# Kernel optimization log

Hardware: AMD Instinct MI355X
Metric: run time of the kernel (lower is better)

## Reference

```python
import jax, jax.numpy as jnp
import numpy as np

N = 50000      # nodes
E = 800000     # edges (before self loops)
D_IN = 128
D_H = 128
HEADS = 4
C = D_H // HEADS
D_OUT = 64
G = 50         # graphs in batch
EPS = 1e-5


def setup_inputs() -> dict:
    key = jax.random.key(0)
    ks = jax.random.split(key, 40)
    def rn(k, shape, scale=0.05):
        return jax.random.normal(k, shape, jnp.float32) * scale
    inp = {}
    inp['x'] = jax.random.normal(ks[0], (N, D_IN), jnp.float32)
    inp['edge_index'] = jax.random.randint(ks[1], (2, E), 0, N, dtype=jnp.int32)
    inp['batch'] = jnp.sort(jax.random.randint(ks[2], (N,), 0, G, dtype=jnp.int32))
    # GATConv 1 (in=D_IN, heads=4, out-per-head=C, concat)
    inp['gat1_W'] = rn(ks[3], (D_IN, D_H))
    inp['gat1_as'] = rn(ks[4], (HEADS, C))
    inp['gat1_ad'] = rn(ks[5], (HEADS, C))
    inp['gat1_b'] = rn(ks[6], (D_H,))
    # GATConv 2 (in=D_H)
    inp['gat2_W'] = rn(ks[7], (D_H, D_H))
    inp['gat2_as'] = rn(ks[8], (HEADS, C))
    inp['gat2_ad'] = rn(ks[9], (HEADS, C))
    inp['gat2_b'] = rn(ks[10], (D_H,))
    # SAGEConv 3/4/5: lin_l (aggregated neighbors, has bias), lin_r (root, no bias)
    for i, kk in zip((3, 4, 5), (11, 14, 17)):
        inp[f'sage{i}_Wl'] = rn(ks[kk], (D_H, D_H))
        inp[f'sage{i}_bl'] = rn(ks[kk + 1], (D_H,))
        inp[f'sage{i}_Wr'] = rn(ks[kk + 2], (D_H, D_H))
    # BatchNorms (training-mode batch statistics)
    for i in range(1, 6):
        inp[f'bn{i}_g'] = jnp.ones((D_H,), jnp.float32)
        inp[f'bn{i}_b'] = jnp.zeros((D_H,), jnp.float32)
    # residual projections + final fc
    inp['res1_W'] = rn(ks[20], (D_IN, D_H)); inp['res1_b'] = rn(ks[21], (D_H,))
    inp['res2_W'] = rn(ks[22], (D_H, D_H)); inp['res2_b'] = rn(ks[23], (D_H,))
    inp['fc_W'] = rn(ks[24], (D_H, D_OUT)); inp['fc_b'] = rn(ks[25], (D_OUT,))
    return inp


def _segsum(v, idx, n):
    return jax.ops.segment_sum(v, idx, num_segments=n)


def _gat(x, W, a_src, a_dst, b, src, dst):
    # PyG GATConv with self loops already appended to (src, dst).
    h = (x @ W).reshape(N, HEADS, C)
    es = jnp.einsum('nhc,hc->nh', h, a_src)           # [N,H]
    ed = jnp.einsum('nhc,hc->nh', h, a_dst)
    e = jax.nn.leaky_relu(es[src] + ed[dst], 0.2)     # [Etot,H]
    m = jax.ops.segment_max(e, dst, num_segments=N)
    m = jnp.where(jnp.isfinite(m), m, 0.0)
    w = jnp.exp(e - m[dst])
    z = _segsum(w, dst, N)
    alpha = w / jnp.maximum(z[dst], 1e-16)            # edge softmax over dst
    out = _segsum(h[src] * alpha[:, :, None], dst, N)  # [N,H,C]
    return out.reshape(N, D_H) + b


def _sage(x, Wl, bl, Wr, src, dst):
    # PyG SAGEConv(aggr='mean'): lin_l(mean_neighbors) + lin_r(x)
    deg = _segsum(jnp.ones((src.shape[0],), x.dtype), dst, N)
    mean = _segsum(x[src], dst, N) / jnp.maximum(deg, 1.0)[:, None]
    return mean @ Wl + bl + x @ Wr


def _bn(x, g, b):
    mu = x.mean(0)
    var = x.var(0)
    return g * (x - mu) * jax.lax.rsqrt(var + EPS) + b


def reference(x, edge_index, batch,
              gat1_W, gat1_as, gat1_ad, gat1_b,
              gat2_W, gat2_as, gat2_ad, gat2_b,
              sage3_Wl, sage3_bl, sage3_Wr,
              sage4_Wl, sage4_bl, sage4_Wr,
              sage5_Wl, sage5_bl, sage5_Wr,
              bn1_g, bn1_b, bn2_g, bn2_b, bn3_g, bn3_b, bn4_g, bn4_b, bn5_g, bn5_b,
              res1_W, res1_b, res2_W, res2_b, fc_W, fc_b):
    src, dst = edge_index[0], edge_index[1]
    loops = jnp.arange(N, dtype=edge_index.dtype)
    gsrc = jnp.concatenate([src, loops])   # GATConv adds self loops by default
    gdst = jnp.concatenate([dst, loops])
    lrelu = lambda v: jax.nn.leaky_relu(v, 0.2)

    res1 = x @ res1_W + res1_b
    h = _gat(x, gat1_W, gat1_as, gat1_ad, gat1_b, gsrc, gdst)
    h = lrelu(_bn(h, bn1_g, bn1_b) + res1)            # dropout = identity (eval)

    res2 = h @ res2_W + res2_b
    h = _gat(h, gat2_W, gat2_as, gat2_ad, gat2_b, gsrc, gdst)
    h = lrelu(_bn(h, bn2_g, bn2_b) + res2)

    h = lrelu(_bn(_sage(h, sage3_Wl, sage3_bl, sage3_Wr, src, dst), bn3_g, bn3_b))
    h = lrelu(_bn(_sage(h, sage4_Wl, sage4_bl, sage4_Wr, src, dst), bn4_g, bn4_b))
    h = lrelu(_bn(_sage(h, sage5_Wl, sage5_bl, sage5_Wr, src, dst), bn5_g, bn5_b))

    # global_mean_pool over graphs
    cnt = jax.ops.segment_sum(jnp.ones((N,), h.dtype), batch, num_segments=G)
    pooled = jax.ops.segment_sum(h, batch, num_segments=G) / jnp.maximum(cnt, 1.0)[:, None]
    return pooled @ fc_W + fc_b
```

## Files before the change

### kernel.cpp

```cpp
#include <hip/hip_runtime.h>
#include <math.h>
#include <stdint.h>

#define N_NODES 50000
#define N_EDGES 800000
#define D 128
#define GR 50
#define EPSV 1e-5f

typedef __attribute__((ext_vector_type(8))) short bf16x8;
typedef __attribute__((ext_vector_type(4))) float f32x4;

__device__ __forceinline__ float lrelu(float v){ return v > 0.f ? v : 0.2f*v; }

__device__ __forceinline__ unsigned int f2bf(float f){
  union { float f; uint32_t i; } v; v.f = f;
  uint32_t r = v.i + 0x7fffu + ((v.i >> 16) & 1u);
  return r >> 16;
}
__device__ __forceinline__ float2 bf2f2(uint32_t u){
  union { uint32_t i; float f; } a, b;
  a.i = u << 16;
  b.i = u & 0xffff0000u;
  return make_float2(a.f, b.f);
}

__global__ void k_countrank(const int* __restrict__ dst, int* __restrict__ deg,
                            int* __restrict__ rank){
  int e = blockIdx.x*256 + threadIdx.x;
  if (e < N_EDGES) rank[e] = atomicAdd(&deg[dst[e]], 1);
}
__global__ void k_scan1(const int* __restrict__ deg, int* __restrict__ bsum){
  __shared__ int s[256];
  int i = blockIdx.x*256 + threadIdx.x;
  int v = (i < N_NODES) ? deg[i] : 0;
  s[threadIdx.x] = v; __syncthreads();
  for (int off = 128; off > 0; off >>= 1){
    if (threadIdx.x < off) s[threadIdx.x] += s[threadIdx.x + off];
    __syncthreads();
  }
  if (threadIdx.x == 0) bsum[blockIdx.x] = s[0];
}
__global__ void k_scan2b(int* __restrict__ bsum, int nb, int* __restrict__ rowStart){
  __shared__ int s[256];
  int t = threadIdx.x;
  int v = (t < nb) ? bsum[t] : 0;
  s[t] = v; __syncthreads();
  for (int off = 1; off < 256; off <<= 1){
    int xv = (t >= off) ? s[t - off] : 0;
    __syncthreads();
    s[t] += xv;
    __syncthreads();
  }
  if (t < nb) bsum[t] = s[t] - v;
  if (t == 255) rowStart[N_NODES] = s[255];
}
__global__ void k_scan3(const int* __restrict__ deg, const int* __restrict__ bsum,
                        int* __restrict__ rowStart){
  __shared__ int s[256];
  int i = blockIdx.x*256 + threadIdx.x;
  int v = (i < N_NODES) ? deg[i] : 0;
  s[threadIdx.x] = v; __syncthreads();
  for (int off = 1; off < 256; off <<= 1){
    int xv = (threadIdx.x >= off) ? s[threadIdx.x - off] : 0;
    __syncthreads();
    s[threadIdx.x] += xv;
    __syncthreads();
  }
  if (i < N_NODES) rowStart[i] = bsum[blockIdx.x] + s[threadIdx.x] - v;
}
__global__ void k_scatter(const int* __restrict__ src, const int* __restrict__ dst,
                          const int* __restrict__ rank, const int* __restrict__ rowStart,
                          int* __restrict__ srcList){
  int e = blockIdx.x*256 + threadIdx.x;
  if (e < N_EDGES)
    srcList[rowStart[dst[e]] + rank[e]] = src[e];
}

__global__ void k_cast_x(const float* __restrict__ x, unsigned short* __restrict__ x16){
  int idx = blockIdx.x*256 + threadIdx.x;
  if (idx >= N_NODES*32) return;
  float4 v = *(const float4*)(x + (size_t)idx*4);
  uint2 pk;
  pk.x = f2bf(v.x) | (f2bf(v.y) << 16);
  pk.y = f2bf(v.z) | (f2bf(v.w) << 16);
  *(uint2*)(x16 + (size_t)idx*4) = pk;
}

struct WPack { const float* w[10]; };
__global__ void k_castw(WPack p, unsigned short* __restrict__ wt){
  int mat = blockIdx.x >> 6;
  int local = (blockIdx.x & 63)*256 + threadIdx.x;
  int c = local >> 7, k = local & 127;
  wt[(size_t)mat*16384 + c*128 + k] = (unsigned short)f2bf(p.w[mat][k*128 + c]);
}

__device__ __forceinline__ void stage_w(const unsigned short* __restrict__ wt,
                                        unsigned short* __restrict__ lds, int t){
  #pragma unroll
  for (int i = 0; i < 8; ++i){
    int ch = i*256 + t;
    int col = ch >> 4, kc = ch & 15;
    *(uint4*)(&lds[col*136 + kc*8]) = *(const uint4*)(wt + ((size_t)col << 7) + (kc << 3));
  }
}

__device__ __forceinline__ void load_a(const unsigned short* __restrict__ xrow,
                                       int quad, bf16x8 a[4]){
  #pragma unroll
  for (int ks = 0; ks < 4; ++ks)
    a[ks] = *(const bf16x8*)(xrow + ks*32 + quad*8);
}

__device__ __forceinline__ void mfma_regs(const bf16x8 a[4],
                                          const unsigned short* __restrict__ lds,
                                          int lane, f32x4 acc[8]){
  int quad = lane >> 4, m = lane & 15;
  #pragma unroll
  for (int ks = 0; ks < 4; ++ks){
    #pragma unroll
    for (int nt = 0; nt < 8; ++nt){
      bf16x8 b = *(const bf16x8*)(&lds[(nt*16 + m)*136 + ks*32 + quad*8]);
      acc[nt] = __builtin_amdgcn_mfma_f32_16x16x32_bf16(a[ks], b, acc[nt], 0, 0, 0);
    }
  }
}

__device__ __forceinline__ void epi_store16(f32x4 acc[8], const float* bias,
    unsigned short* __restrict__ ldsw, unsigned short* __restrict__ Y16,
    int rbase, int lane, int n){
  int quad = lane >> 4, m = lane & 15;
  #pragma unroll
  for (int nt = 0; nt < 8; ++nt){
    int col = nt*16 + m;
    float bv = bias ? bias[col] : 0.f;
    #pragma unroll
    for (int reg = 0; reg < 4; ++reg)
      ldsw[(quad*4 + reg)*132 + col] = (unsigned short)f2bf(acc[nt][reg] + bv);
  }
  int r = lane >> 2, seg = lane & 3;
  int grow = rbase + r;
  if (grow < n){
    unsigned short* gp = Y16 + (size_t)grow*128 + seg*32;
    #pragma unroll
    for (int j = 0; j < 4; ++j)
      *(uint4*)(gp + j*8) = *(const uint4*)(&ldsw[r*132 + seg*32 + j*8]);
  }
}

__global__ __launch_bounds__(256) void k_mgemm_dual(const unsigned short* __restrict__ X16,
    const unsigned short* __restrict__ wtres, const unsigned short* __restrict__ wtgat,
    const float* __restrict__ bres, const float* __restrict__ as_,
    const float* __restrict__ ad_, unsigned short* __restrict__ R16,
    unsigned short* __restrict__ H16, float* __restrict__ es, float* __restrict__ ed,
    int n){
  __shared__ __align__(16) unsigned short Wlds[128*136];
  int t = threadIdx.x, lane = t & 63, w = t >> 6;
  int quad = lane >> 4, m = lane & 15;
  int rbase = blockIdx.x*64 + w*16;
  int rowA = rbase + m; if (rowA >= n) rowA = n - 1;
  bf16x8 a[4];
  load_a(X16 + (size_t)rowA*128, quad, a);
  stage_w(wtres, Wlds, t);
  f32x4 accR[8], accG[8];
  #pragma unroll
  for (int nt = 0; nt < 8; ++nt){
    accR[nt][0]=0.f; accR[nt][1]=0.f; accR[nt][2]=0.f; accR[nt][3]=0.f;
    accG[nt][0]=0.f; accG[nt][1]=0.f; accG[nt][2]=0.f; accG[nt][3]=0.f;
  }
  __syncthreads();
  mfma_regs(a, Wlds, lane, accR);
  __syncthreads();
  stage_w(wtgat, Wlds, t);
  __syncthreads();
  mfma_regs(a, Wlds, lane, accG);

  float asv[8], adv[8];
  #pragma unroll
  for (int nt = 0; nt < 8; ++nt){ asv[nt] = as_[nt*16 + m]; adv[nt] = ad_[nt*16 + m]; }
  #pragma unroll
  for (int reg = 0; reg < 4; ++reg){
    int row = rbase + quad*4 + reg;
    float pe[4], pd[4];
    #pragma unroll
    for (int h = 0; h < 4; ++h){
      pe[h] = accG[2*h][reg]*asv[2*h] + accG[2*h+1][reg]*asv[2*h+1];
      pd[h] = accG[2*h][reg]*adv[2*h] + accG[2*h+1][reg]*adv[2*h+1];
    }
    #pragma unroll
    for (int h = 0; h < 4; ++h){
      pe[h] += __shfl_xor(pe[h], 1); pe[h] += __shfl_xor(pe[h], 2);
      pe[h] += __shfl_xor(pe[h], 4); pe[h] += __shfl_xor(pe[h], 8);
      pd[h] += __shfl_xor(pd[h], 1); pd[h] += __shfl_xor(pd[h], 2);
      pd[h] += __shfl_xor(pd[h], 4); pd[h] += __shfl_xor(pd[h], 8);
    }
    if (m == 0 && row < n){
      #pragma unroll
      for (int h = 0; h < 4; ++h){ es[row*4 + h] = pe[h]; ed[row*4 + h] = pd[h]; }
    }
  }
  __syncthreads();
  epi_store16(accR, bres,    Wlds + w*2112, R16, rbase, lane, n);
  epi_store16(accG, nullptr, Wlds + w*2112, H16, rbase, lane, n);
}

__global__ __launch_bounds__(256) void k_mgemm2(const unsigned short* __restrict__ Xa,
    const unsigned short* __restrict__ wta, const unsigned short* __restrict__ Xb,
    const unsigned short* __restrict__ wtb, const float* __restrict__ bias,
    unsigned short* __restrict__ Y16, int n, float* __restrict__ bnpart){
  __shared__ __align__(16) unsigned short Wlds[128*136];
  __shared__ float wredS[4][128], wredQ[4][128];
  int t = threadIdx.x, lane = t & 63, w = t >> 6;
  int quad = lane >> 4, m = lane & 15;
  int rbase = blockIdx.x*64 + w*16;
  int rowA = rbase + m; if (rowA >= n) rowA = n - 1;
  bf16x8 aa[4], ab[4];
  load_a(Xa + (size_t)rowA*128, quad, aa);
  load_a(Xb + (size_t)rowA*128, quad, ab);
  stage_w(wta, Wlds, t);
  f32x4 acc[8];
  #pragma unroll
  for (int nt = 0; nt < 8; ++nt){ acc[nt][0]=0.f; acc[nt][1]=0.f; acc[nt][2]=0.f; acc[nt][3]=0.f; }
  __syncthreads();
  mfma_regs(aa, Wlds, lane, acc);
  __syncthreads();
  stage_w(wtb, Wlds, t);
  __syncthreads();
  mfma_regs(ab, Wlds, lane, acc);

  float colS[8], colQ[8];
  #pragma unroll
  for (int nt = 0; nt < 8; ++nt){
    float bv = bias[nt*16 + m];
    float s = 0.f, q = 0.f;
    #pragma unroll
    for (int reg = 0; reg < 4; ++reg){
      float o = acc[nt][reg] + bv;
      acc[nt][reg] = o;
      if (rbase + quad*4 + reg < n){ s += o; q += o*o; }
    }
    s += __shfl_xor(s, 16); s += __shfl_xor(s, 32);
    q += __shfl_xor(q, 16); q += __shfl_xor(q, 32);
    colS[nt] = s; colQ[nt] = q;
  }
  if (quad == 0){
    #pragma unroll
    for (int nt = 0; nt < 8; ++nt){
      wredS[w][nt*16 + m] = colS[nt];
      wredQ[w][nt*16 + m] = colQ[nt];
    }
  }
  __syncthreads();
  if (t < 128){
    float S = wredS[0][t] + wredS[1][t] + wredS[2][t] + wredS[3][t];
    float Q = wredQ[0][t] + wredQ[1][t] + wredQ[2][t] + wredQ[3][t];
    bnpart[(size_t)blockIdx.x*256 + t]       = S;
    bnpart[(size_t)blockIdx.x*256 + 128 + t] = Q;
  }
  epi_store16(acc, nullptr, Wlds + w*2112, Y16, rbase, lane, n);
}

__global__ void k_bnred(const float* __restrict__ part, int nblk,
                        float* __restrict__ sums){
  int g = blockIdx.x, t = threadIdx.x;
  int chunk = (nblk + 63) / 64;
  int b0 = g*chunk, b1 = min(nblk, b0 + chunk);
  float s = 0.f;
  for (int b = b0; b < b1; ++b) s += part[(size_t)b*256 + t];
  if (b0 < b1) atomicAdd(&sums[t], s);
}

__global__ __launch_bounds__(256) void k_gat(const uint4* __restrict__ h16,
    const float* __restrict__ es, const float* __restrict__ edv,
    const int* __restrict__ rowStart, const int* __restrict__ srcList,
    const float* __restrict__ bias, uint4* __restrict__ out16){
  int i = blockIdx.x*4 + (threadIdx.x >> 6);
  if (i >= N_NODES) return;
  int lane = threadIdx.x & 63;
  int sub = lane >> 4;
  int m   = lane & 15;
  int hd  = m >> 2;
  float edi = edv[i*4 + hd];
  float acc[8];
  #pragma unroll
  for (int j = 0; j < 8; ++j) acc[j] = 0.f;
  float z = 0.f;
  if (sub == 0){
    float ws = __expf(lrelu(es[i*4 + hd] + edi));
    uint4 u = h16[i*16 + m];
    float2 v0=bf2f2(u.x), v1=bf2f2(u.y), v2=bf2f2(u.z), v3=bf2f2(u.w);
    acc[0]=v0.x*ws; acc[1]=v0.y*ws; acc[2]=v1.x*ws; acc[3]=v1.y*ws;
    acc[4]=v2.x*ws; acc[5]=v2.y*ws; acc[6]=v3.x*ws; acc[7]=v3.y*ws;
    z = ws;
  }
  int k0 = rowStart[i], ke = rowStart[i + 1];
  for (int k = k0; k < ke; k += 8){
    int e0 = k + sub, e1 = k + 4 + sub;
    int c0 = e0 < ke ? e0 : ke - 1;
    int c1 = e1 < ke ? e1 : ke - 1;
    int s0 = srcList[c0];
    int s1 = srcList[c1];
    uint4 u0 = h16[s0*16 + m];
    uint4 u1 = h16[s1*16 + m];
    float w0 = (e0 < ke) ? __expf(lrelu(es[s0*4 + hd] + edi)) : 0.f;
    float w1 = (e1 < ke) ? __expf(lrelu(es[s1*4 + hd] + edi)) : 0.f;
    z += w0 + w1;
    float2 a0=bf2f2(u0.x), a1=bf2f2(u0.y), a2=bf2f2(u0.z), a3=bf2f2(u0.w);
    float2 b0=bf2f2(u1.x), b1=bf2f2(u1.y), b2=bf2f2(u1.z), b3=bf2f2(u1.w);
    acc[0] += a0.x*w0 + b0.x*w1;  acc[1] += a0.y*w0 + b0.y*w1;
    acc[2] += a1.x*w0 + b1.x*w1;  acc[3] += a1.y*w0 + b1.y*w1;
    acc[4] += a2.x*w0 + b2.x*w1;  acc[5] += a2.y*w0 + b2.y*w1;
    acc[6] += a3.x*w0 + b3.x*w1;  acc[7] += a3.y*w0 + b3.y*w1;
  }
  #pragma unroll
  for (int j = 0; j < 8; ++j){
    acc[j] += __shfl_xor(acc[j], 16);
    acc[j] += __shfl_xor(acc[j], 32);
  }
  z += __shfl_xor(z, 16);
  z += __shfl_xor(z, 32);
  if (sub == 0){
    float inv = 1.f / z;
    float4 bv0 = *(const float4*)(bias + m*8);
    float4 bv1 = *(const float4*)(bias + m*8 + 4);
    uint4 pk;
    pk.x = f2bf(acc[0]*inv + bv0.x) | (f2bf(acc[1]*inv + bv0.y) << 16);
    pk.y = f2bf(acc[2]*inv + bv0.z) | (f2bf(acc[3]*inv + bv0.w) << 16);
    pk.z = f2bf(acc[4]*inv + bv1.x) | (f2bf(acc[5]*inv + bv1.y) << 16);
    pk.w = f2bf(acc[6]*inv + bv1.z) | (f2bf(acc[7]*inv + bv1.w) << 16);
    out16[i*16 + m] = pk;
  }
}

__global__ __launch_bounds__(256) void k_sage_mean(const uint4* __restrict__ h16,
    const int* __restrict__ rowStart, const int* __restrict__ srcList,
    uint4* __restrict__ out16){
  int i = blockIdx.x*4 + (threadIdx.x >> 6);
  if (i >= N_NODES) return;
  int lane = threadIdx.x & 63;
  int sub = lane >> 4;
  int m   = lane & 15;
  float acc[8];
  #pragma unroll
  for (int j = 0; j < 8; ++j) acc[j] = 0.f;
  int k0 = rowStart[i], ke = rowStart[i + 1];
  for (int k = k0; k < ke; k += 8){
    int e0 = k + sub, e1 = k + 4 + sub;
    int c0 = e0 < ke ? e0 : ke - 1;
    int c1 = e1 < ke ? e1 : ke - 1;
    int s0 = srcList[c0];
    int s1 = srcList[c1];
    uint4 u0 = h16[s0*16 + m];
    uint4 u1 = h16[s1*16 + m];
    float w0 = (e0 < ke) ? 1.f : 0.f;
    float w1 = (e1 < ke) ? 1.f : 0.f;
    float2 a0=bf2f2(u0.x), a1=bf2f2(u0.y), a2=bf2f2(u0.z), a3=bf2f2(u0.w);
    float2 b0=bf2f2(u1.x), b1=bf2f2(u1.y), b2=bf2f2(u1.z), b3=bf2f2(u1.w);
    acc[0] += a0.x*w0 + b0.x*w1;  acc[1] += a0.y*w0 + b0.y*w1;
    acc[2] += a1.x*w0 + b1.x*w1;  acc[3] += a1.y*w0 + b1.y*w1;
    acc[4] += a2.x*w0 + b2.x*w1;  acc[5] += a2.y*w0 + b2.y*w1;
    acc[6] += a3.x*w0 + b3.x*w1;  acc[7] += a3.y*w0 + b3.y*w1;
  }
  #pragma unroll
  for (int j = 0; j < 8; ++j){
    acc[j] += __shfl_xor(acc[j], 16);
    acc[j] += __shfl_xor(acc[j], 32);
  }
  if (sub == 0){
    int dg = ke - k0;
    float inv = 1.f / (float)(dg > 0 ? dg : 1);
    uint4 pk;
    pk.x = f2bf(acc[0]*inv) | (f2bf(acc[1]*inv) << 16);
    pk.y = f2bf(acc[2]*inv) | (f2bf(acc[3]*inv) << 16);
    pk.z = f2bf(acc[4]*inv) | (f2bf(acc[5]*inv) << 16);
    pk.w = f2bf(acc[6]*inv) | (f2bf(acc[7]*inv) << 16);
    out16[i*16 + m] = pk;
  }
}

__global__ __launch_bounds__(256) void k_bnstat(const unsigned int* __restrict__ x16,
                                                float* __restrict__ sums){
  int colu = threadIdx.x & 63;
  int ro   = threadIdx.x >> 6;
  float s0 = 0.f, s1 = 0.f, q0 = 0.f, q1 = 0.f;
  for (int r = blockIdx.x*4 + ro; r < N_NODES; r += gridDim.x*4){
    float2 v = bf2f2(x16[(size_t)r*64 + colu]);
    s0 += v.x; s1 += v.y; q0 += v.x*v.x; q1 += v.y*v.y;
  }
  __shared__ float rs0[256], rs1[256], rq0[256], rq1[256];
  int t = threadIdx.x;
  rs0[t] = s0; rs1[t] = s1; rq0[t] = q0; rq1[t] = q1;
  __syncthreads();
  if (t < 64){
    float S0 = rs0[t] + rs0[t+64] + rs0[t+128] + rs0[t+192];
    float S1 = rs1[t] + rs1[t+64] + rs1[t+128] + rs1[t+192];
    float Q0 = rq0[t] + rq0[t+64] + rq0[t+128] + rq0[t+192];
    float Q1 = rq1[t] + rq1[t+64] + rq1[t+128] + rq1[t+192];
    atomicAdd(&sums[2*t],       S0);
    atomicAdd(&sums[2*t + 1],   S1);
    atomicAdd(&sums[128 + 2*t],     Q0);
    atomicAdd(&sums[128 + 2*t + 1], Q1);
  }
}

__global__ void k_bnapply(const unsigned int* __restrict__ x16,
    const float* __restrict__ sums, const float* __restrict__ g,
    const float* __restrict__ b, const unsigned int* __restrict__ res16,
    unsigned int* __restrict__ y16){
  int f = blockIdx.x*256 + threadIdx.x;
  if (f >= N_NODES*32) return;
  int c = (f & 31) * 4;
  uint2 u = *(const uint2*)(x16 + (size_t)f*2);
  float2 vA = bf2f2(u.x), vB = bf2f2(u.y);
  float vv[4] = {vA.x, vA.y, vB.x, vB.y};
  float rr[4] = {0.f, 0.f, 0.f, 0.f};
  if (res16){
    uint2 ur = *(const uint2*)(res16 + (size_t)f*2);
    float2 rA = bf2f2(ur.x), rB = bf2f2(ur.y);
    rr[0]=rA.x; rr[1]=rA.y; rr[2]=rB.x; rr[3]=rB.y;
  }
  float o[4];
  const float invn = 1.f / (float)N_NODES;
  #pragma unroll
  for (int j = 0; j < 4; ++j){
    int cc = c + j;
    float mu  = sums[cc] * invn;
    float var = sums[128 + cc] * invn - mu*mu;
    float rs  = rsqrtf(var + EPSV);
    o[j] = lrelu((vv[j] - mu)*rs*g[cc] + b[cc] + rr[j]);
  }
  uint2 pk;
  pk.x = f2bf(o[0]) | (f2bf(o[1]) << 16);
  pk.y = f2bf(o[2]) | (f2bf(o[3]) << 16);
  *(uint2*)(y16 + (size_t)f*2) = pk;
}

__global__ __launch_bounds__(256) void k_pool(const unsigned int* __restrict__ h16,
    const int* __restrict__ batch, float* __restrict__ pooled,
    float* __restrict__ cnt){
  int colu = threadIdx.x & 63;
  int ro   = threadIdx.x >> 6;
  int base = blockIdx.x * 128;
  int g_cur = -1; float a0 = 0.f, a1 = 0.f, cacc = 0.f;
  for (int ii = 0; ii < 32; ++ii){
    int r = base + ro + ii*4;
    if (r >= N_NODES) break;
    int g = batch[r];
    if (g != g_cur){
      if (g_cur >= 0){
        atomicAdd(&pooled[g_cur*D + 2*colu],     a0);
        atomicAdd(&pooled[g_cur*D + 2*colu + 1], a1);
        if (colu == 0) atomicAdd(&cnt[g_cur], cacc);
      }
      a0 = 0.f; a1 = 0.f; cacc = 0.f; g_cur = g;
    }
    float2 v = bf2f2(h16[(size_t)r*64 + colu]);
    a0 += v.x; a1 += v.y; cacc += 1.f;
  }
  if (g_cur >= 0){
    atomicAdd(&pooled[g_cur*D + 2*colu],     a0);
    atomicAdd(&pooled[g_cur*D + 2*colu + 1], a1);
    if (colu == 0) atomicAdd(&cnt[g_cur], cacc);
  }
}

__global__ void k_fc(const float* __restrict__ pooled, const float* __restrict__ cnt,
    const float* __restrict__ W, const float* __restrict__ b, float* __restrict__ out){
  int idx = blockIdx.x*256 + threadIdx.x;
  if (idx >= GR*64) return;
  int g = idx >> 6, o = idx & 63;
  const float* p = pooled + g*D;
  float s = 0.f;
  for (int c2 = 0; c2 < D; ++c2) s += p[c2] * W[c2*64 + o];
  float inv = 1.f / fmaxf(cnt[g], 1.f);
  out[idx] = s*inv + b[o];
}

extern "C" void kernel_launch(void* const* d_in, const int* in_sizes, int n_in,
                              void* d_out, int out_size, void* d_ws, size_t ws_size,
                              hipStream_t stream){
  (void)in_sizes; (void)n_in; (void)out_size; (void)ws_size;
  const float* x       = (const float*)d_in[0];
  const int*   ei      = (const int*)  d_in[1];
  const int*   batch   = (const int*)  d_in[2];
  const float* gat1_W  = (const float*)d_in[3];
  const float* gat1_as = (const float*)d_in[4];
  const float* gat1_ad = (const float*)d_in[5];
  const float* gat1_b  = (const float*)d_in[6];
  const float* gat2_W  = (const float*)d_in[7];
  const float* gat2_as = (const float*)d_in[8];
  const float* gat2_ad = (const float*)d_in[9];
  const float* gat2_b  = (const float*)d_in[10];
  const float* s3_Wl   = (const float*)d_in[11];
  const float* s3_bl   = (const float*)d_in[12];
  const float* s3_Wr   = (const float*)d_in[13];
  const float* s4_Wl   = (const float*)d_in[14];
  const float* s4_bl   = (const float*)d_in[15];
  const float* s4_Wr   = (const float*)d_in[16];
  const float* s5_Wl   = (const float*)d_in[17];
  const float* s5_bl   = (const float*)d_in[18];
  const float* s5_Wr   = (const float*)d_in[19];
  const float* bn1_g = (const float*)d_in[20]; const float* bn1_b = (const float*)d_in[21];
  const float* bn2_g = (const float*)d_in[22]; const float* bn2_b = (const float*)d_in[23];
  const float* bn3_g = (const float*)d_in[24]; const float* bn3_b = (const float*)d_in[25];
  const float* bn4_g = (const float*)d_in[26]; const float* bn4_b = (const float*)d_in[27];
  const float* bn5_g = (const float*)d_in[28]; const float* bn5_b = (const float*)d_in[29];
  const float* res1_W = (const float*)d_in[30]; const float* res1_b = (const float*)d_in[31];
  const float* res2_W = (const float*)d_in[32]; const float* res2_b = (const float*)d_in[33];
  const float* fc_W   = (const float*)d_in[34]; const float* fc_b   = (const float*)d_in[35];
  float* out = (float*)d_out;

  char* ws = (char*)d_ws;
  size_t off = 0;
  auto alloc = [&](size_t bytes) -> void* {
    void* p = ws + off; off += (bytes + 255) & ~(size_t)255; return p;
  };
  const int mgrid = (N_NODES + 63) / 64;
  int*   rowStart = (int*)  alloc((N_NODES + 1) * 4);
  int*   deg      = (int*)  alloc((size_t)N_NODES * 4);
  int*   rank     = (int*)  alloc((size_t)N_EDGES * 4);
  int*   srcList  = (int*)  alloc((size_t)N_EDGES * 4);
  int*   bsum     = (int*)  alloc(256 * 4);
  float* bnsums   = (float*)alloc(5 * 256 * 4);
  float* pooled   = (float*)alloc(GR * D * 4);
  float* cnt      = (float*)alloc(64 * 4);
  float* es       = (float*)alloc((size_t)N_NODES * 4 * 4);
  float* edv      = (float*)alloc((size_t)N_NODES * 4 * 4);
  float* bnpart   = (float*)alloc((size_t)mgrid * 256 * 4);
  unsigned short* Wt16 = (unsigned short*)alloc(10 * 16384 * 2);
  unsigned short* HX   = (unsigned short*)alloc((size_t)N_NODES * D * 2);
  unsigned short* H16a = (unsigned short*)alloc((size_t)N_NODES * D * 2);
  unsigned short* HO   = (unsigned short*)alloc((size_t)N_NODES * D * 2);
  unsigned short* HR   = (unsigned short*)alloc((size_t)N_NODES * D * 2);

  const int* srcE = ei;
  const int* dstE = ei + N_EDGES;
  const int nb = (N_NODES + 255) / 256;
  const int egrid = (N_EDGES + 255) / 256;
  const int agrid = (N_NODES + 3) / 4;
  const int bgrid = (N_NODES*32 + 255) / 256;
  const int pgrid = (N_NODES + 127) / 128;

  hipMemsetAsync(deg, 0, (size_t)N_NODES*4, stream);
  hipMemsetAsync(bnsums, 0, (5*256 + GR*D + 64)*4, stream);
  k_countrank<<<egrid, 256, 0, stream>>>(dstE, deg, rank);
  k_scan1<<<nb, 256, 0, stream>>>(deg, bsum);
  k_scan2b<<<1, 256, 0, stream>>>(bsum, nb, rowStart);
  k_scan3<<<nb, 256, 0, stream>>>(deg, bsum, rowStart);
  k_scatter<<<egrid, 256, 0, stream>>>(srcE, dstE, rank, rowStart, srcList);

  WPack wp;
  wp.w[0]=res1_W; wp.w[1]=gat1_W; wp.w[2]=res2_W; wp.w[3]=gat2_W;
  wp.w[4]=s3_Wl;  wp.w[5]=s3_Wr;  wp.w[6]=s4_Wl;  wp.w[7]=s4_Wr;
  wp.w[8]=s5_Wl;  wp.w[9]=s5_Wr;
  k_castw<<<640, 256, 0, stream>>>(wp, Wt16);
  k_cast_x<<<bgrid, 256, 0, stream>>>(x, HX);

  k_mgemm_dual<<<mgrid, 256, 0, stream>>>(HX, Wt16 + 0*16384, Wt16 + 1*16384,
                                          res1_b, gat1_as, gat1_ad,
                                          HR, H16a, es, edv, N_NODES);
  k_gat<<<agrid, 256, 0, stream>>>((const uint4*)H16a, es, edv, rowStart,
                                   srcList, gat1_b, (uint4*)HO);
  k_bnstat<<<256, 256, 0, stream>>>((const unsigned int*)HO, bnsums);
  k_bnapply<<<bgrid, 256, 0, stream>>>((const unsigned int*)HO, bnsums, bn1_g, bn1_b,
                                       (const unsigned int*)HR, (unsigned int*)H16a);

  k_mgemm_dual<<<mgrid, 256, 0, stream>>>(H16a, Wt16 + 2*16384, Wt16 + 3*16384,
                                          res2_b, gat2_as, gat2_ad,
                                          HR, HX, es, edv, N_NODES);
  k_gat<<<agrid, 256, 0, stream>>>((const uint4*)HX, es, edv, rowStart,
                                   srcList, gat2_b, (uint4*)HO);
  k_bnstat<<<256, 256, 0, stream>>>((const unsigned int*)HO, bnsums + 256);
  k_bnapply<<<bgrid, 256, 0, stream>>>((const unsigned int*)HO, bnsums + 256, bn2_g, bn2_b,
                                       (const unsigned int*)HR, (unsigned int*)H16a);

  k_sage_mean<<<agrid, 256, 0, stream>>>((const uint4*)H16a, rowStart, srcList,
                                         (uint4*)HX);
  k_mgemm2<<<mgrid, 256, 0, stream>>>(HX, Wt16 + 4*16384, H16a, Wt16 + 5*16384,
                                      s3_bl, HO, N_NODES, bnpart);
  k_bnred<<<64, 256, 0, stream>>>(bnpart, mgrid, bnsums + 512);
  k_bnapply<<<bgrid, 256, 0, stream>>>((const unsigned int*)HO, bnsums + 512, bn3_g, bn3_b,
                                       nullptr, (unsigned int*)H16a);

  k_sage_mean<<<agrid, 256, 0, stream>>>((const uint4*)H16a, rowStart, srcList,
                                         (uint4*)HX);
  k_mgemm2<<<mgrid, 256, 0, stream>>>(HX, Wt16 + 6*16384, H16a, Wt16 + 7*16384,
                                      s4_bl, HO, N_NODES, bnpart);
  k_bnred<<<64, 256, 0, stream>>>(bnpart, mgrid, bnsums + 768);
  k_bnapply<<<bgrid, 256, 0, stream>>>((const unsigned int*)HO, bnsums + 768, bn4_g, bn4_b,
                                       nullptr, (unsigned int*)H16a);

  k_sage_mean<<<agrid, 256, 0, stream>>>((const uint4*)H16a, rowStart, srcList,
                                         (uint4*)HX);
  k_mgemm2<<<mgrid, 256, 0, stream>>>(HX, Wt16 + 8*16384, H16a, Wt16 + 9*16384,
                                      s5_bl, HO, N_NODES, bnpart);
  k_bnred<<<64, 256, 0, stream>>>(bnpart, mgrid, bnsums + 1024);
  k_bnapply<<<bgrid, 256, 0, stream>>>((const unsigned int*)HO, bnsums + 1024, bn5_g, bn5_b,
                                       nullptr, (unsigned int*)H16a);

  k_pool<<<pgrid, 256, 0, stream>>>((const unsigned int*)H16a, batch, pooled, cnt);
  k_fc<<<(GR*64 + 255)/256, 256, 0, stream>>>(pooled, cnt, fc_W, fc_b, out);
}
```

Measured before the change: 614.7 us.

## Merge cast kernels, fuse pool with fc, peel gather tail, single memset

Combines the weight and input bf16 cast kernels into one launch. Fuses global mean pooling with the final fc using a last-block atomic counter. Splits the GAT and SAGE neighbor gather loops into an unguarded main loop plus one tail iteration. Reorders workspace allocations so a single memset clears all zero-initialized buffers. The aim is fewer launches and less per-edge bounds work, at the cost of a serial fc computed by one block at the end.

```diff
diff --git a/kernel.cpp b/kernel.cpp
--- a/kernel.cpp
+++ b/kernel.cpp
@@ -77,22 +77,24 @@
     srcList[rowStart[dst[e]] + rank[e]] = src[e];
 }
 
-__global__ void k_cast_x(const float* __restrict__ x, unsigned short* __restrict__ x16){
-  int idx = blockIdx.x*256 + threadIdx.x;
-  if (idx >= N_NODES*32) return;
-  float4 v = *(const float4*)(x + (size_t)idx*4);
-  uint2 pk;
-  pk.x = f2bf(v.x) | (f2bf(v.y) << 16);
-  pk.y = f2bf(v.z) | (f2bf(v.w) << 16);
-  *(uint2*)(x16 + (size_t)idx*4) = pk;
-}
-
 struct WPack { const float* w[10]; };
-__global__ void k_castw(WPack p, unsigned short* __restrict__ wt){
-  int mat = blockIdx.x >> 6;
-  int local = (blockIdx.x & 63)*256 + threadIdx.x;
-  int c = local >> 7, k = local & 127;
-  wt[(size_t)mat*16384 + c*128 + k] = (unsigned short)f2bf(p.w[mat][k*128 + c]);
+__global__ void k_casts(WPack p, unsigned short* __restrict__ wt,
+                        const float* __restrict__ x, unsigned short* __restrict__ x16){
+  int b = blockIdx.x;
+  if (b < 640){
+    int mat = b >> 6;
+    int local = (b & 63)*256 + threadIdx.x;
+    int c = local >> 7, k = local & 127;
+    wt[(size_t)mat*16384 + c*128 + k] = (unsigned short)f2bf(p.w[mat][k*128 + c]);
+  } else {
+    int idx = (b - 640)*256 + threadIdx.x;
+    if (idx >= N_NODES*32) return;
+    float4 v = *(const float4*)(x + (size_t)idx*4);
+    uint2 pk;
+    pk.x = f2bf(v.x) | (f2bf(v.y) << 16);
+    pk.y = f2bf(v.z) | (f2bf(v.w) << 16);
+    *(uint2*)(x16 + (size_t)idx*4) = pk;
+  }
 }
 
 __device__ __forceinline__ void stage_w(const unsigned short* __restrict__ wt,
@@ -294,7 +296,24 @@
     z = ws;
   }
   int k0 = rowStart[i], ke = rowStart[i + 1];
-  for (int k = k0; k < ke; k += 8){
+  int kfull = k0 + ((ke - k0) & ~7);
+  int k = k0;
+  for (; k < kfull; k += 8){
+    int s0 = srcList[k + sub];
+    int s1 = srcList[k + 4 + sub];
+    uint4 u0 = h16[s0*16 + m];
+    uint4 u1 = h16[s1*16 + m];
+    float w0 = __expf(lrelu(es[s0*4 + hd] + edi));
+    float w1 = __expf(lrelu(es[s1*4 + hd] + edi));
+    z += w0 + w1;
+    float2 a0=bf2f2(u0.x), a1=bf2f2(u0.y), a2=bf2f2(u0.z), a3=bf2f2(u0.w);
+    float2 b0=bf2f2(u1.x), b1=bf2f2(u1.y), b2=bf2f2(u1.z), b3=bf2f2(u1.w);
+    acc[0] += a0.x*w0 + b0.x*w1;  acc[1] += a0.y*w0 + b0.y*w1;
+    acc[2] += a1.x*w0 + b1.x*w1;  acc[3] += a1.y*w0 + b1.y*w1;
+    acc[4] += a2.x*w0 + b2.x*w1;  acc[5] += a2.y*w0 + b2.y*w1;
+    acc[6] += a3.x*w0 + b3.x*w1;  acc[7] += a3.y*w0 + b3.y*w1;
+  }
+  if (k < ke){
     int e0 = k + sub, e1 = k + 4 + sub;
     int c0 = e0 < ke ? e0 : ke - 1;
     int c1 = e1 < ke ? e1 : ke - 1;
@@ -344,7 +363,21 @@
   #pragma unroll
   for (int j = 0; j < 8; ++j) acc[j] = 0.f;
   int k0 = rowStart[i], ke = rowStart[i + 1];
-  for (int k = k0; k < ke; k += 8){
+  int kfull = k0 + ((ke - k0) & ~7);
+  int k = k0;
+  for (; k < kfull; k += 8){
+    int s0 = srcList[k + sub];
+    int s1 = srcList[k + 4 + sub];
+    uint4 u0 = h16[s0*16 + m];
+    uint4 u1 = h16[s1*16 + m];
+    float2 a0=bf2f2(u0.x), a1=bf2f2(u0.y), a2=bf2f2(u0.z), a3=bf2f2(u0.w);
+    float2 b0=bf2f2(u1.x), b1=bf2f2(u1.y), b2=bf2f2(u1.z), b3=bf2f2(u1.w);
+    acc[0] += a0.x + b0.x;  acc[1] += a0.y + b0.y;
+    acc[2] += a1.x + b1.x;  acc[3] += a1.y + b1.y;
+    acc[4] += a2.x + b2.x;  acc[5] += a2.y + b2.y;
+    acc[6] += a3.x + b3.x;  acc[7] += a3.y + b3.y;
+  }
+  if (k < ke){
     int e0 = k + sub, e1 = k + 4 + sub;
     int c0 = e0 < ke ? e0 : ke - 1;
     int c1 = e1 < ke ? e1 : ke - 1;
@@ -435,9 +468,11 @@
   *(uint2*)(y16 + (size_t)f*2) = pk;
 }
 
-__global__ __launch_bounds__(256) void k_pool(const unsigned int* __restrict__ h16,
+__global__ __launch_bounds__(256) void k_pool_fc(const unsigned int* __restrict__ h16,
     const int* __restrict__ batch, float* __restrict__ pooled,
-    float* __restrict__ cnt){
+    float* __restrict__ cnt, int* __restrict__ pctr,
+    const float* __restrict__ W, const float* __restrict__ bfc,
+    float* __restrict__ out){
   int colu = threadIdx.x & 63;
   int ro   = threadIdx.x >> 6;
   int base = blockIdx.x * 128;
@@ -462,18 +497,22 @@
     atomicAdd(&pooled[g_cur*D + 2*colu + 1], a1);
     if (colu == 0) atomicAdd(&cnt[g_cur], cacc);
   }
-}
-
-__global__ void k_fc(const float* __restrict__ pooled, const float* __restrict__ cnt,
-    const float* __restrict__ W, const float* __restrict__ b, float* __restrict__ out){
-  int idx = blockIdx.x*256 + threadIdx.x;
-  if (idx >= GR*64) return;
-  int g = idx >> 6, o = idx & 63;
-  const float* p = pooled + g*D;
-  float s = 0.f;
-  for (int c2 = 0; c2 < D; ++c2) s += p[c2] * W[c2*64 + o];
-  float inv = 1.f / fmaxf(cnt[g], 1.f);
-  out[idx] = s*inv + b[o];
+  __threadfence();
+  __shared__ int isLast;
+  if (threadIdx.x == 0)
+    isLast = (atomicAdd(pctr, 1) == (int)gridDim.x - 1);
+  __syncthreads();
+  if (isLast){
+    __threadfence();
+    for (int idx = threadIdx.x; idx < GR*64; idx += 256){
+      int g = idx >> 6, o = idx & 63;
+      const float* p = pooled + g*D;
+      float s = 0.f;
+      for (int c2 = 0; c2 < D; ++c2) s += p[c2] * W[c2*64 + o];
+      float inv = 1.f / fmaxf(cnt[g], 1.f);
+      out[idx] = s*inv + bfc[o];
+    }
+  }
 }
 
 extern "C" void kernel_launch(void* const* d_in, const int* in_sizes, int n_in,
@@ -517,13 +556,16 @@
   };
   const int mgrid = (N_NODES + 63) / 64;
   int*   rowStart = (int*)  alloc((N_NODES + 1) * 4);
-  int*   deg      = (int*)  alloc((size_t)N_NODES * 4);
   int*   rank     = (int*)  alloc((size_t)N_EDGES * 4);
   int*   srcList  = (int*)  alloc((size_t)N_EDGES * 4);
   int*   bsum     = (int*)  alloc(256 * 4);
+  size_t zoff0 = off;
+  int*   deg      = (int*)  alloc((size_t)N_NODES * 4);
   float* bnsums   = (float*)alloc(5 * 256 * 4);
   float* pooled   = (float*)alloc(GR * D * 4);
   float* cnt      = (float*)alloc(64 * 4);
+  int*   pctr     = (int*)  alloc(4);
+  size_t zbytes = off - zoff0;
   float* es       = (float*)alloc((size_t)N_NODES * 4 * 4);
   float* edv      = (float*)alloc((size_t)N_NODES * 4 * 4);
   float* bnpart   = (float*)alloc((size_t)mgrid * 256 * 4);
@@ -541,8 +583,7 @@
   const int bgrid = (N_NODES*32 + 255) / 256;
   const int pgrid = (N_NODES + 127) / 128;
 
-  hipMemsetAsync(deg, 0, (size_t)N_NODES*4, stream);
-  hipMemsetAsync(bnsums, 0, (5*256 + GR*D + 64)*4, stream);
+  hipMemsetAsync(ws + zoff0, 0, zbytes, stream);
   k_countrank<<<egrid, 256, 0, stream>>>(dstE, deg, rank);
   k_scan1<<<nb, 256, 0, stream>>>(deg, bsum);
   k_scan2b<<<1, 256, 0, stream>>>(bsum, nb, rowStart);
@@ -553,8 +594,7 @@
   wp.w[0]=res1_W; wp.w[1]=gat1_W; wp.w[2]=res2_W; wp.w[3]=gat2_W;
   wp.w[4]=s3_Wl;  wp.w[5]=s3_Wr;  wp.w[6]=s4_Wl;  wp.w[7]=s4_Wr;
   wp.w[8]=s5_Wl;  wp.w[9]=s5_Wr;
-  k_castw<<<640, 256, 0, stream>>>(wp, Wt16);
-  k_cast_x<<<bgrid, 256, 0, stream>>>(x, HX);
+  k_casts<<<640 + bgrid, 256, 0, stream>>>(wp, Wt16, x, HX);
 
   k_mgemm_dual<<<mgrid, 256, 0, stream>>>(HX, Wt16 + 0*16384, Wt16 + 1*16384,
                                           res1_b, gat1_as, gat1_ad,
@@ -598,6 +638,6 @@
   k_bnapply<<<bgrid, 256, 0, stream>>>((const unsigned int*)HO, bnsums + 1024, bn5_g, bn5_b,
                                        nullptr, (unsigned int*)H16a);
 
-  k_pool<<<pgrid, 256, 0, stream>>>((const unsigned int*)H16a, batch, pooled, cnt);
-  k_fc<<<(GR*64 + 255)/256, 256, 0, stream>>>(pooled, cnt, fc_W, fc_b, out);
-}
+  k_pool_fc<<<pgrid, 256, 0, stream>>>((const unsigned int*)H16a, batch, pooled, cnt,
+                                       pctr, fc_W, fc_b, out);
+}
```

Result: slower. 649.2 us (+5.6%).
